# Kernel optimization log

Measured on AMD Instinct MI355X. Metric: run time of the kernel, lower is better.

Reference implementation:

```python
import jax, jax.numpy as jnp
import numpy as np

TOK_DIM = 512
POS_DIM = 512
N_HEADS = 16
HEAD_DIM = 64
D_MODEL = 1024
INNER = N_HEADS * HEAD_DIM
B, T = 4, 2048


def setup_inputs() -> dict:
    key = jax.random.key(0)
    ks = jax.random.split(key, 5)
    s = 0.02
    return {
        "x": jax.random.normal(ks[0], (B, T, TOK_DIM + POS_DIM), dtype=jnp.float32),
        "Wq": jax.random.normal(ks[1], (POS_DIM, INNER), dtype=jnp.float32) * s,
        "Wk": jax.random.normal(ks[2], (POS_DIM, INNER), dtype=jnp.float32) * s,
        "Wv": jax.random.normal(ks[3], (TOK_DIM, INNER), dtype=jnp.float32) * s,
        "Wo": jax.random.normal(ks[4], (INNER, D_MODEL), dtype=jnp.float32) * s,
    }


def reference(x, Wq, Wk, Wv, Wo):
    b, t, _ = x.shape
    x_tok = x[:, :, :TOK_DIM]
    x_pos = x[:, :, TOK_DIM:]
    # project and split heads: [B, H, T, Dh]
    q = (x_pos @ Wq).reshape(b, t, N_HEADS, HEAD_DIM).transpose(0, 2, 1, 3)
    k = (x_pos @ Wk).reshape(b, t, N_HEADS, HEAD_DIM).transpose(0, 2, 1, 3)
    v = (x_tok @ Wv).reshape(b, t, N_HEADS, HEAD_DIM).transpose(0, 2, 1, 3)
    att = jnp.einsum("bhqd,bhkd->bhqk", q, k) / jnp.sqrt(jnp.float32(HEAD_DIM))
    causal = jnp.tril(jnp.ones((t, t), dtype=bool))
    att = jnp.where(causal, att, -jnp.inf)
    att = jax.nn.softmax(att, axis=-1)
    out = jnp.einsum("bhqk,bhkd->bhqd", att, v)
    out = out.transpose(0, 2, 1, 3).reshape(b, t, INNER)
    return out @ Wo
```

## Files before the change

### kernel.cpp

```cpp
#include <hip/hip_runtime.h>
#include <stdint.h>


typedef unsigned short u16;
typedef __bf16 bf16;
typedef bf16 bf16x8 __attribute__((ext_vector_type(8)));
typedef u16 u16x8 __attribute__((ext_vector_type(8)));
typedef u16 u16x4 __attribute__((ext_vector_type(4)));
typedef float f32x4 __attribute__((ext_vector_type(4)));
typedef uint32_t u32x4 __attribute__((ext_vector_type(4)));

__device__ __forceinline__ u16 cvt_bf16(float f) {
  uint32_t u = __builtin_bit_cast(uint32_t, f);
  u += 0x7FFFu + ((u >> 16) & 1u);
  return (u16)(u >> 16);
}

__device__ __forceinline__ uint32_t pack2_bf16(float lo, float hi) {
  uint32_t a = __builtin_bit_cast(uint32_t, lo) + 0x8000u;
  uint32_t b = __builtin_bit_cast(uint32_t, hi) + 0x8000u;
  return __builtin_amdgcn_perm(b, a, 0x07060302u);
}

__device__ __forceinline__ f32x4 mfma_bf(bf16x8 a, bf16x8 b, f32x4 c) {
  return __builtin_amdgcn_mfma_f32_16x16x32_bf16(a, b, c, 0, 0, 0);
}

typedef __attribute__((address_space(1))) const uint32_t g_u32;
typedef __attribute__((address_space(3))) uint32_t l_u32;
__device__ __forceinline__ void gload16(const u16* g, u16* l) {
  __builtin_amdgcn_global_load_lds((g_u32*)g, (l_u32*)l, 16, 0, 0);
}

__global__ __launch_bounds__(256) void prep_x(
    const float* __restrict__ x, u16* __restrict__ xtok,
    u16* __restrict__ xpos) {
  int idx = blockIdx.x * 256 + threadIdx.x;
  int row = idx >> 8;
  int c4 = (idx & 255) * 4;
  float4 v = *(const float4*)(x + (size_t)row * 1024 + c4);
  u16x4 b = {cvt_bf16(v.x), cvt_bf16(v.y), cvt_bf16(v.z), cvt_bf16(v.w)};
  u16* dst = (c4 < 512) ? (xtok + (size_t)row * 512 + c4)
                        : (xpos + (size_t)row * 512 + c4 - 512);
  *(u16x4*)dst = b;
}

__global__ __launch_bounds__(256) void prep_w(
    const float* __restrict__ Wq, const float* __restrict__ Wk,
    const float* __restrict__ Wv, const float* __restrict__ Wo,
    u16* __restrict__ Wt, u16* __restrict__ WoT) {
  const int z = blockIdx.z;
  const float* src = (z == 0) ? Wq : (z == 1) ? Wk : (z == 2) ? Wv : Wo;
  const int K = (z == 3) ? 1024 : 512;
  u16* dst = (z == 3) ? WoT : (Wt + (size_t)z * 1024 * 512);
  const int k0 = blockIdx.y * 64, n0 = blockIdx.x * 64;
  if (k0 >= K) return;
  __shared__ u16 T[64][68];
  const int tid = threadIdx.x;
  const int r = tid >> 4, c = (tid & 15) * 4;
#pragma unroll
  for (int i = 0; i < 4; i++) {
    float4 v = *(const float4*)(src + (size_t)(k0 + r + i * 16) * 1024 + n0 + c);
    u16x4 b = {cvt_bf16(v.x), cvt_bf16(v.y), cvt_bf16(v.z), cvt_bf16(v.w)};
    *(u16x4*)&T[r + i * 16][c] = b;
  }
  __syncthreads();
#pragma unroll
  for (int i = 0; i < 4; i++) {
    int n = r + i * 16;
    u16x4 v;
#pragma unroll
    for (int j = 0; j < 4; j++) v[j] = T[c + j][n];
    *(u16x4*)(dst + (size_t)(n0 + n) * K + k0 + c) = v;
  }
}

__global__ __launch_bounds__(256) void gemm_qkv(
    const u16* __restrict__ xtok, const u16* __restrict__ xpos,
    const u16* __restrict__ Wt, u16* __restrict__ qkv,
    u16* __restrict__ vperm) {
  const int z = blockIdx.z;
  const u16* A = (z == 2) ? xtok : xpos;
  const u16* Bt = Wt + (size_t)z * 1024 * 512;
  u16* outp = qkv + (size_t)z * (64u * 2048u * 64u);
  const float osc = (z == 0) ? 0.18033688011112042f : 1.0f;

  const int m0 = blockIdx.y * 128;
  const int n0 = blockIdx.x * 128;
  const int tid = threadIdx.x;
  const int lane = tid & 63;
  const int w = tid >> 6;
  const int wm = (w & 1) * 64;
  const int wn = (w >> 1) * 64;
  const int mrow = lane & 15;
  const int quad = lane >> 4;

  __shared__ __align__(16) u16 Ash[128 * 32];
  __shared__ __align__(16) u16 Bsh[128 * 32];

  f32x4 acc[4][4];
#pragma unroll
  for (int i = 0; i < 4; i++)
#pragma unroll
    for (int j = 0; j < 4; j++) acc[i][j] = (f32x4){0.f, 0.f, 0.f, 0.f};

  const int sr = w * 16 + (lane >> 2);
  const int sc = (lane & 3) * 8;
  const u16* gA = A + (size_t)(m0 + sr) * 512 + sc;
  const u16* gB = Bt + (size_t)(n0 + sr) * 512 + sc;
  u16* lA = Ash + sr * 32 + sc;
  u16* lB = Bsh + sr * 32 + sc;

  for (int kb = 0; kb < 512; kb += 32) {
    __syncthreads();
    gload16(gA + kb, lA);
    gload16(gA + 64 * 512 + kb, lA + 64 * 32);
    gload16(gB + kb, lB);
    gload16(gB + 64 * 512 + kb, lB + 64 * 32);
    __syncthreads();

    bf16x8 af[4], bfr[4];
#pragma unroll
    for (int mi = 0; mi < 4; mi++)
      af[mi] = *(const bf16x8*)(Ash + (wm + mi * 16 + mrow) * 32 + quad * 8);
#pragma unroll
    for (int ni = 0; ni < 4; ni++)
      bfr[ni] = *(const bf16x8*)(Bsh + (wn + ni * 16 + mrow) * 32 + quad * 8);
#pragma unroll
    for (int mi = 0; mi < 4; mi++)
#pragma unroll
      for (int ni = 0; ni < 4; ni++)
        acc[mi][ni] = mfma_bf(af[mi], bfr[ni], acc[mi][ni]);
  }

  if (z != 2) {
#pragma unroll
    for (int mi = 0; mi < 4; mi++)
#pragma unroll
      for (int ni = 0; ni < 4; ni++)
#pragma unroll
        for (int r = 0; r < 4; r++) {
          int m = m0 + wm + mi * 16 + quad * 4 + r;
          int n = n0 + wn + ni * 16 + mrow;
          int bb = m >> 11, t = m & 2047;
          int h = n >> 6, d = n & 63;
          outp[(((size_t)(bb * 16 + h)) * 2048 + t) * 64 + d] =
              cvt_bf16(acc[mi][ni][r] * osc);
        }
  } else {
#pragma unroll
    for (int mi = 0; mi < 4; mi++)
#pragma unroll
      for (int ni = 0; ni < 4; ni++)
#pragma unroll
        for (int r = 0; r < 4; r++) {
          int m = m0 + wm + mi * 16 + quad * 4 + r;
          int n = n0 + wn + ni * 16 + mrow;
          int bb = m >> 11, t = m & 2047;
          int h = n >> 6, d = n & 63;
          int k6 = t & 63;
          int pos = (k6 & 32) + ((k6 >> 4) & 1) * 4 + ((k6 >> 2) & 3) * 8 +
                    (k6 & 3);
          vperm[(((size_t)(bb * 16 + h)) * 64 + d) * 2048 + (t & ~63) + pos] =
              cvt_bf16(acc[mi][ni][r]);
        }
  }
}

__global__ __launch_bounds__(256, 2) void attn(
    const u16* __restrict__ qkv, const u16* __restrict__ vperm,
    u16* __restrict__ aout) {
  const int bh = blockIdx.x;
  const int sp = blockIdx.y;
  const int bb = bh >> 4, h = bh & 15;
  const u16* Qp = qkv + (size_t)bh * (2048 * 64);
  const u16* Kp = qkv + (size_t)(64 + bh) * (2048 * 64);
  const u16* Vp = vperm + (size_t)bh * (64 * 2048);

  __shared__ __align__(16) u16 Ksh0[64 * 32], Ksh1[64 * 32];
  __shared__ __align__(16) u16 Vsh0[64 * 32], Vsh1[64 * 32];
  __shared__ __align__(16) u16 Osh[4][32][72];

  const int tid = threadIdx.x;
  const int lane = tid & 63;
  const int w = tid >> 6;
  const int mrow = lane & 15;
  const int quad = lane >> 4;
  const int srow = w * 16 + (lane >> 2);
  const int sc = (lane & 3) * 8;

  const u16x8 onesu = {0x3F80, 0x3F80, 0x3F80, 0x3F80,
                       0x3F80, 0x3F80, 0x3F80, 0x3F80};
  const bf16x8 ones = __builtin_bit_cast(bf16x8, onesu);

  const u16* kgb = Kp + (size_t)srow * 64 + sc;
  const u16* vgb = Vp + (size_t)srow * 2048 + sc;

  for (int half = 0; half < 2; ++half) {
    const int qt = (half == 0) ? sp : 15 - sp;
    const int q0 = qt * 128;
    const int nk = 2 * qt + 2;
    const int qw = q0 + w * 32;

    const u16* qbase = Qp + (size_t)(qw + mrow) * 64 + quad * 8;
    const bf16x8 qf00 = *(const bf16x8*)qbase;
    const bf16x8 qf01 = *(const bf16x8*)(qbase + 32);
    const bf16x8 qf10 = *(const bf16x8*)(qbase + 16 * 64);
    const bf16x8 qf11 = *(const bf16x8*)(qbase + 16 * 64 + 32);

    f32x4 o[2][4], ol[2];
#pragma unroll
    for (int g = 0; g < 2; ++g) {
#pragma unroll
      for (int dt = 0; dt < 4; ++dt) o[g][dt] = (f32x4){0.f, 0.f, 0.f, 0.f};
      ol[g] = (f32x4){0.f, 0.f, 0.f, 0.f};
    }

    u16x8 ka0 = *(const u16x8*)kgb;
    u16x8 ka1 = *(const u16x8*)(kgb + 32);
    u16x8 va0 = *(const u16x8*)vgb;
    u16x8 va1 = *(const u16x8*)(vgb + 32);

    for (int it = 0; it < nk; ++it) {
      __syncthreads();
      *(u16x8*)(Ksh0 + srow * 32 + sc) = ka0;
      *(u16x8*)(Ksh1 + srow * 32 + sc) = ka1;
      *(u16x8*)(Vsh0 + srow * 32 + sc) = va0;
      *(u16x8*)(Vsh1 + srow * 32 + sc) = va1;
      __syncthreads();

      if (it + 1 < nk) {
        const int kn = (it + 1) * 64;
        ka0 = *(const u16x8*)(kgb + (size_t)kn * 64);
        ka1 = *(const u16x8*)(kgb + (size_t)kn * 64 + 32);
        va0 = *(const u16x8*)(vgb + kn);
        va1 = *(const u16x8*)(vgb + kn + 32);
      }

      const int k0 = it * 64;
      if (k0 > qw + 31) continue;

      f32x4 s[2][4];
#pragma unroll
      for (int nt = 0; nt < 4; ++nt) {
        bf16x8 kf0 = *(const bf16x8*)(Ksh0 + (nt * 16 + mrow) * 32 + quad * 8);
        bf16x8 kf1 = *(const bf16x8*)(Ksh1 + (nt * 16 + mrow) * 32 + quad * 8);
        f32x4 z0 = (f32x4){0.f, 0.f, 0.f, 0.f};
        z0 = mfma_bf(kf0, qf00, z0);
        s[0][nt] = mfma_bf(kf1, qf01, z0);
        f32x4 z1 = (f32x4){0.f, 0.f, 0.f, 0.f};
        z1 = mfma_bf(kf0, qf10, z1);
        s[1][nt] = mfma_bf(kf1, qf11, z1);
      }

      if (k0 + 63 > qw) {
#pragma unroll
        for (int g = 0; g < 2; ++g)
#pragma unroll
          for (int nt = 0; nt < 4; ++nt)
#pragma unroll
            for (int r = 0; r < 4; ++r)
              if (k0 + nt * 16 + quad * 4 + r > qw + g * 16 + mrow)
                s[g][nt][r] = -1e30f;
      }
#pragma unroll
      for (int g = 0; g < 2; ++g)
#pragma unroll
        for (int nt = 0; nt < 4; ++nt)
#pragma unroll
          for (int r = 0; r < 4; ++r)
            s[g][nt][r] = __builtin_amdgcn_exp2f(s[g][nt][r]);

      bf16x8 pf[2][2];
#pragma unroll
      for (int g = 0; g < 2; ++g) {
        u32x4 pw0 = {pack2_bf16(s[g][0][0], s[g][0][1]),
                     pack2_bf16(s[g][0][2], s[g][0][3]),
                     pack2_bf16(s[g][1][0], s[g][1][1]),
                     pack2_bf16(s[g][1][2], s[g][1][3])};
        u32x4 pw1 = {pack2_bf16(s[g][2][0], s[g][2][1]),
                     pack2_bf16(s[g][2][2], s[g][2][3]),
                     pack2_bf16(s[g][3][0], s[g][3][1]),
                     pack2_bf16(s[g][3][2], s[g][3][3])};
        pf[g][0] = __builtin_bit_cast(bf16x8, pw0);
        pf[g][1] = __builtin_bit_cast(bf16x8, pw1);
        ol[g] = mfma_bf(ones, pf[g][0], ol[g]);
        ol[g] = mfma_bf(ones, pf[g][1], ol[g]);
      }

#pragma unroll
      for (int dt = 0; dt < 4; ++dt) {
        bf16x8 vf0 = *(const bf16x8*)(Vsh0 + (dt * 16 + mrow) * 32 + quad * 8);
        bf16x8 vf1 = *(const bf16x8*)(Vsh1 + (dt * 16 + mrow) * 32 + quad * 8);
        o[0][dt] = mfma_bf(vf0, pf[0][0], o[0][dt]);
        o[0][dt] = mfma_bf(vf1, pf[0][1], o[0][dt]);
        o[1][dt] = mfma_bf(vf0, pf[1][0], o[1][dt]);
        o[1][dt] = mfma_bf(vf1, pf[1][1], o[1][dt]);
      }
    }

#pragma unroll
    for (int g = 0; g < 2; ++g) {
      const float inv = 1.f / ol[g][0];
#pragma unroll
      for (int dt = 0; dt < 4; ++dt)
#pragma unroll
        for (int r = 0; r < 4; ++r)
          Osh[w][g * 16 + mrow][dt * 16 + quad * 4 + r] =
              cvt_bf16(o[g][dt][r] * inv);
    }
#pragma unroll
    for (int p = 0; p < 4; ++p) {
      int ql = (lane >> 3) + 8 * p;
      int ch = lane & 7;
      u16x8 v = *(const u16x8*)&Osh[w][ql][ch * 8];
      int t = q0 + w * 32 + ql;
      *(u16x8*)(aout + ((size_t)(bb * 2048 + t)) * 1024 + h * 64 + ch * 8) = v;
    }
  }
}

__global__ __launch_bounds__(256) void gemm_out(
    const u16* __restrict__ Am, const u16* __restrict__ WoT,
    float* __restrict__ out) {
  const int m0 = blockIdx.y * 128;
  const int n0 = blockIdx.x * 128;
  const int tid = threadIdx.x;
  const int lane = tid & 63;
  const int w = tid >> 6;
  const int wm = (w & 1) * 64;
  const int wn = (w >> 1) * 64;
  const int mrow = lane & 15;
  const int quad = lane >> 4;

  __shared__ __align__(16) u16 Ash[128 * 32];
  __shared__ __align__(16) u16 Bsh[128 * 32];

  f32x4 acc[4][4];
#pragma unroll
  for (int i = 0; i < 4; i++)
#pragma unroll
    for (int j = 0; j < 4; j++) acc[i][j] = (f32x4){0.f, 0.f, 0.f, 0.f};

  const int sr = w * 16 + (lane >> 2);
  const int sc = (lane & 3) * 8;
  const u16* gA = Am + (size_t)(m0 + sr) * 1024 + sc;
  const u16* gB = WoT + (size_t)(n0 + sr) * 1024 + sc;
  u16* lA = Ash + sr * 32 + sc;
  u16* lB = Bsh + sr * 32 + sc;

  for (int kb = 0; kb < 1024; kb += 32) {
    __syncthreads();
    gload16(gA + kb, lA);
    gload16(gA + 64 * 1024 + kb, lA + 64 * 32);
    gload16(gB + kb, lB);
    gload16(gB + 64 * 1024 + kb, lB + 64 * 32);
    __syncthreads();

    bf16x8 af[4], bfr[4];
#pragma unroll
    for (int mi = 0; mi < 4; mi++)
      af[mi] = *(const bf16x8*)(Ash + (wm + mi * 16 + mrow) * 32 + quad * 8);
#pragma unroll
    for (int ni = 0; ni < 4; ni++)
      bfr[ni] = *(const bf16x8*)(Bsh + (wn + ni * 16 + mrow) * 32 + quad * 8);
#pragma unroll
    for (int mi = 0; mi < 4; mi++)
#pragma unroll
      for (int ni = 0; ni < 4; ni++)
        acc[mi][ni] = mfma_bf(af[mi], bfr[ni], acc[mi][ni]);
  }

#pragma unroll
  for (int mi = 0; mi < 4; mi++)
#pragma unroll
    for (int ni = 0; ni < 4; ni++)
#pragma unroll
      for (int r = 0; r < 4; r++) {
        int m = m0 + wm + mi * 16 + quad * 4 + r;
        int n = n0 + wn + ni * 16 + mrow;
        out[(size_t)m * 1024 + n] = acc[mi][ni][r];
      }
}

extern "C" void kernel_launch(void* const* d_in, const int* in_sizes, int n_in,
                              void* d_out, int out_size, void* d_ws, size_t ws_size,
                              hipStream_t stream) {
  const float* x  = (const float*)d_in[0];
  const float* Wq = (const float*)d_in[1];
  const float* Wk = (const float*)d_in[2];
  const float* Wv = (const float*)d_in[3];
  const float* Wo = (const float*)d_in[4];

  u16* qkv   = (u16*)d_ws;
  u16* vperm = qkv + (size_t)3 * 64 * 2048 * 64;
  u16* aout  = vperm + (size_t)64 * 64 * 2048;
  u16* xtok  = aout + (size_t)8192 * 1024;
  u16* xpos  = xtok + (size_t)8192 * 512;
  u16* Wt    = xpos + (size_t)8192 * 512;
  u16* WoT   = Wt + (size_t)3 * 1024 * 512;
  float* out = (float*)d_out;

  prep_x<<<dim3(8192), dim3(256), 0, stream>>>(x, xtok, xpos);
  prep_w<<<dim3(16, 16, 4), dim3(256), 0, stream>>>(Wq, Wk, Wv, Wo, Wt, WoT);
  gemm_qkv<<<dim3(8, 64, 3), dim3(256), 0, stream>>>(xtok, xpos, Wt, qkv, vperm);
  attn<<<dim3(64, 8), dim3(256), 0, stream>>>(qkv, vperm, aout);
  gemm_out<<<dim3(8, 64), dim3(256), 0, stream>>>(aout, WoT, out);
}
```

Measured before the change: 215.3 us.

## Replace QKV and output GEMMs with 256x256 pipelined, swizzled 8-wave GEMM core

Both projection GEMMs now share a 256x256-tile core run by 512 threads. It uses K-step 64, double-buffered LDS with XOR-swizzled layout, and interleaved global-to-LDS loads issued between MFMA phases. Raw s_barrier and s_waitcnt calls plus setprio are used in place of __syncthreads. The goal is more data reuse per tile, fewer LDS bank conflicts, and load latency hidden behind compute. In exchange it uses 128KB LDS per block, heavy register use from 32 accumulators, and fewer blocks (384 for QKV, 128 for the output GEMM), which may leave CUs idle on the smaller GEMM.

```diff
diff --git a/kernel.cpp b/kernel.cpp
--- a/kernel.cpp
+++ b/kernel.cpp
@@ -75,7 +75,113 @@
   }
 }
 
-__global__ __launch_bounds__(256) void gemm_qkv(
+
+#define LDA(P, S) { const u16* bp_ = rA + (P)*16384 + (S)*8192;              \
+  af[0][0] = *(const bf16x8*)(bp_ + 0*1024 + colx0);                         \
+  af[0][1] = *(const bf16x8*)(bp_ + 0*1024 + colx1);                         \
+  af[1][0] = *(const bf16x8*)(bp_ + 1*1024 + colx0);                         \
+  af[1][1] = *(const bf16x8*)(bp_ + 1*1024 + colx1);                         \
+  af[2][0] = *(const bf16x8*)(bp_ + 2*1024 + colx0);                         \
+  af[2][1] = *(const bf16x8*)(bp_ + 2*1024 + colx1);                         \
+  af[3][0] = *(const bf16x8*)(bp_ + 3*1024 + colx0);                         \
+  af[3][1] = *(const bf16x8*)(bp_ + 3*1024 + colx1); }
+
+#define LDB(P, S, NB) { const u16* bp_ = rB + (P)*16384 + (S)*8192;          \
+  bf[(NB)+0][0] = *(const bf16x8*)(bp_ + 0*1024 + colx0);                    \
+  bf[(NB)+0][1] = *(const bf16x8*)(bp_ + 0*1024 + colx1);                    \
+  bf[(NB)+1][0] = *(const bf16x8*)(bp_ + 1*1024 + colx0);                    \
+  bf[(NB)+1][1] = *(const bf16x8*)(bp_ + 1*1024 + colx1); }
+
+#define MM1(M_, N_, J_) { f32x4 c_ = acc[M_][N_];                            \
+  c_ = mfma_bf(af[J_][0], bf[N_][0], c_);                                    \
+  c_ = mfma_bf(af[J_][1], bf[N_][1], c_);                                    \
+  acc[M_][N_] = c_; }
+
+#define MM(MB, NB) MM1((MB)+0,(NB)+0,0) MM1((MB)+0,(NB)+1,0)                 \
+                   MM1((MB)+1,(NB)+0,1) MM1((MB)+1,(NB)+1,1)                 \
+                   MM1((MB)+2,(NB)+0,2) MM1((MB)+2,(NB)+1,2)                 \
+                   MM1((MB)+3,(NB)+0,3) MM1((MB)+3,(NB)+1,3)
+
+#define STA(P, S, KT) { const u16* s_ = gA + (size_t)(S)*64*Kd + (KT)*64;    \
+  u16* d_ = lA + (P)*16384 + (S)*8192;                                       \
+  gload16(s_, d_); gload16(s_ + (size_t)128*Kd, d_ + 4096); }
+
+#define STB(P, S, KT) { const u16* s_ = gB + (size_t)(S)*32*Kd + (KT)*64;    \
+  u16* d_ = lB + (P)*16384 + (S)*8192;                                       \
+  gload16(s_, d_); gload16(s_ + (size_t)128*Kd, d_ + 4096); }
+
+#define PH_MID  asm volatile("" ::: "memory"); __builtin_amdgcn_s_barrier(); \
+  asm volatile("s_waitcnt lgkmcnt(0)" ::: "memory");                         \
+  __builtin_amdgcn_s_setprio(1);
+
+#define PH_END  __builtin_amdgcn_s_setprio(0);                               \
+  asm volatile("" ::: "memory"); __builtin_amdgcn_s_barrier();
+
+#define PH_END_VM  __builtin_amdgcn_s_setprio(0);                            \
+  asm volatile("s_waitcnt vmcnt(6)" ::: "memory");                           \
+  asm volatile("" ::: "memory"); __builtin_amdgcn_s_barrier();
+
+template <int Kd>
+__device__ __forceinline__ void gemm256_core(
+    const u16* __restrict__ Aptr, const u16* __restrict__ Bptr,
+    int m0, int n0, u16* smem, f32x4 (&acc)[8][4]) {
+  constexpr int NKT = Kd / 64;
+  constexpr int NI = NKT / 2;
+  const int tid = threadIdx.x;
+  const int lane = tid & 63;
+  const int mrow = lane & 15, quad = lane >> 4;
+  const int w = tid >> 6, wm2 = w >> 2, wn4 = w & 3;
+
+  u16* As = smem;
+  u16* Bs = smem + 32768;
+
+  const int lrs = tid >> 3, sp8 = tid & 7;
+  const int slog = sp8 ^ (lrs & 7);
+  const u16* gA = Aptr + (size_t)(m0 + (lrs & 63)) * Kd + slog * 8;
+  const u16* gB =
+      Bptr + (size_t)(n0 + ((lrs >> 5) << 6) + (lrs & 31)) * Kd + slog * 8;
+  u16* lA = As + tid * 8;
+  u16* lB = Bs + tid * 8;
+
+  const int colx0 = (quad * 8) ^ ((mrow & 7) * 8);
+  const int colx1 = (32 + quad * 8) ^ ((mrow & 7) * 8);
+  const u16* rA = As + (wm2 * 64 + mrow) * 64;
+  const u16* rB = Bs + (wn4 * 32 + mrow) * 64;
+
+  bf16x8 af[4][2], bf[4][2];
+
+  STA(0, 0, 0) STB(0, 0, 0) STB(0, 1, 0) STA(0, 1, 0)
+  STA(1, 0, 1) STB(1, 0, 1) STB(1, 1, 1)
+  asm volatile("s_waitcnt vmcnt(6)" ::: "memory");
+  asm volatile("" ::: "memory");
+  __builtin_amdgcn_s_barrier();
+
+  for (int i = 0; i < NI; ++i) {
+    const int kt1 = 2 * i + 1;
+    const int kt2 = (2 * i + 2 < NKT) ? 2 * i + 2 : NKT - 1;
+    const int kt3 = (2 * i + 3 < NKT) ? 2 * i + 3 : NKT - 1;
+    LDA(0, 0) LDB(0, 0, 0) STA(1, 1, kt1)
+    PH_MID MM(0, 0) PH_END
+    LDB(0, 1, 2) STA(0, 0, kt2)
+    PH_MID MM(0, 2) PH_END
+    LDA(0, 1) STB(0, 0, kt2)
+    PH_MID MM(4, 2) PH_END
+    STB(0, 1, kt2)
+    PH_MID MM(4, 0) PH_END_VM
+    LDA(1, 0) LDB(1, 0, 0) STA(0, 1, kt2)
+    PH_MID MM(0, 0) PH_END
+    LDB(1, 1, 2) STA(1, 0, kt3)
+    PH_MID MM(0, 2) PH_END
+    LDA(1, 1) STB(1, 0, kt3)
+    PH_MID MM(4, 2) PH_END
+    STB(1, 1, kt3)
+    PH_MID MM(4, 0) PH_END_VM
+  }
+  asm volatile("s_waitcnt vmcnt(0)" ::: "memory");
+  __builtin_amdgcn_s_barrier();
+}
+
+__global__ __launch_bounds__(512, 2) void gemm_qkv256(
     const u16* __restrict__ xtok, const u16* __restrict__ xpos,
     const u16* __restrict__ Wt, u16* __restrict__ qkv,
     u16* __restrict__ vperm) {
@@ -84,64 +190,31 @@
   const u16* Bt = Wt + (size_t)z * 1024 * 512;
   u16* outp = qkv + (size_t)z * (64u * 2048u * 64u);
   const float osc = (z == 0) ? 0.18033688011112042f : 1.0f;
-
-  const int m0 = blockIdx.y * 128;
-  const int n0 = blockIdx.x * 128;
+  const int m0 = blockIdx.y * 256, n0 = blockIdx.x * 256;
+
+  __shared__ __align__(16) u16 smem[65536];
+  f32x4 acc[8][4];
+#pragma unroll
+  for (int i = 0; i < 8; i++)
+#pragma unroll
+    for (int j = 0; j < 4; j++) acc[i][j] = (f32x4){0.f, 0.f, 0.f, 0.f};
+
+  gemm256_core<512>(A, Bt, m0, n0, smem, acc);
+
   const int tid = threadIdx.x;
   const int lane = tid & 63;
-  const int w = tid >> 6;
-  const int wm = (w & 1) * 64;
-  const int wn = (w >> 1) * 64;
-  const int mrow = lane & 15;
-  const int quad = lane >> 4;
-
-  __shared__ __align__(16) u16 Ash[128 * 32];
-  __shared__ __align__(16) u16 Bsh[128 * 32];
-
-  f32x4 acc[4][4];
-#pragma unroll
-  for (int i = 0; i < 4; i++)
-#pragma unroll
-    for (int j = 0; j < 4; j++) acc[i][j] = (f32x4){0.f, 0.f, 0.f, 0.f};
-
-  const int sr = w * 16 + (lane >> 2);
-  const int sc = (lane & 3) * 8;
-  const u16* gA = A + (size_t)(m0 + sr) * 512 + sc;
-  const u16* gB = Bt + (size_t)(n0 + sr) * 512 + sc;
-  u16* lA = Ash + sr * 32 + sc;
-  u16* lB = Bsh + sr * 32 + sc;
-
-  for (int kb = 0; kb < 512; kb += 32) {
-    __syncthreads();
-    gload16(gA + kb, lA);
-    gload16(gA + 64 * 512 + kb, lA + 64 * 32);
-    gload16(gB + kb, lB);
-    gload16(gB + 64 * 512 + kb, lB + 64 * 32);
-    __syncthreads();
-
-    bf16x8 af[4], bfr[4];
-#pragma unroll
-    for (int mi = 0; mi < 4; mi++)
-      af[mi] = *(const bf16x8*)(Ash + (wm + mi * 16 + mrow) * 32 + quad * 8);
-#pragma unroll
-    for (int ni = 0; ni < 4; ni++)
-      bfr[ni] = *(const bf16x8*)(Bsh + (wn + ni * 16 + mrow) * 32 + quad * 8);
-#pragma unroll
-    for (int mi = 0; mi < 4; mi++)
+  const int mrow = lane & 15, quad = lane >> 4;
+  const int w = tid >> 6, wm2 = w >> 2, wn4 = w & 3;
+
+  if (z != 2) {
+#pragma unroll
+    for (int mi = 0; mi < 8; mi++)
 #pragma unroll
       for (int ni = 0; ni < 4; ni++)
-        acc[mi][ni] = mfma_bf(af[mi], bfr[ni], acc[mi][ni]);
-  }
-
-  if (z != 2) {
-#pragma unroll
-    for (int mi = 0; mi < 4; mi++)
-#pragma unroll
-      for (int ni = 0; ni < 4; ni++)
 #pragma unroll
         for (int r = 0; r < 4; r++) {
-          int m = m0 + wm + mi * 16 + quad * 4 + r;
-          int n = n0 + wn + ni * 16 + mrow;
+          int m = m0 + wm2 * 128 + mi * 16 + quad * 4 + r;
+          int n = n0 + wn4 * 64 + ni * 16 + mrow;
           int bb = m >> 11, t = m & 2047;
           int h = n >> 6, d = n & 63;
           outp[(((size_t)(bb * 16 + h)) * 2048 + t) * 64 + d] =
@@ -149,13 +222,13 @@
         }
   } else {
 #pragma unroll
-    for (int mi = 0; mi < 4; mi++)
+    for (int mi = 0; mi < 8; mi++)
 #pragma unroll
       for (int ni = 0; ni < 4; ni++)
 #pragma unroll
         for (int r = 0; r < 4; r++) {
-          int m = m0 + wm + mi * 16 + quad * 4 + r;
-          int n = n0 + wn + ni * 16 + mrow;
+          int m = m0 + wm2 * 128 + mi * 16 + quad * 4 + r;
+          int n = n0 + wn4 * 64 + ni * 16 + mrow;
           int bb = m >> 11, t = m & 2047;
           int h = n >> 6, d = n & 63;
           int k6 = t & 63;
@@ -165,6 +238,37 @@
               cvt_bf16(acc[mi][ni][r]);
         }
   }
+}
+
+__global__ __launch_bounds__(512, 2) void gemm_out256(
+    const u16* __restrict__ Am, const u16* __restrict__ WoT,
+    float* __restrict__ out) {
+  const int m0 = blockIdx.y * 256, n0 = blockIdx.x * 256;
+
+  __shared__ __align__(16) u16 smem[65536];
+  f32x4 acc[8][4];
+#pragma unroll
+  for (int i = 0; i < 8; i++)
+#pragma unroll
+    for (int j = 0; j < 4; j++) acc[i][j] = (f32x4){0.f, 0.f, 0.f, 0.f};
+
+  gemm256_core<1024>(Am, WoT, m0, n0, smem, acc);
+
+  const int tid = threadIdx.x;
+  const int lane = tid & 63;
+  const int mrow = lane & 15, quad = lane >> 4;
+  const int w = tid >> 6, wm2 = w >> 2, wn4 = w & 3;
+
+#pragma unroll
+  for (int mi = 0; mi < 8; mi++)
+#pragma unroll
+    for (int ni = 0; ni < 4; ni++)
+#pragma unroll
+      for (int r = 0; r < 4; r++) {
+        int m = m0 + wm2 * 128 + mi * 16 + quad * 4 + r;
+        int n = n0 + wn4 * 64 + ni * 16 + mrow;
+        out[(size_t)m * 1024 + n] = acc[mi][ni][r];
+      }
 }
 
 __global__ __launch_bounds__(256, 2) void attn(
@@ -320,69 +424,6 @@
   }
 }
 
-__global__ __launch_bounds__(256) void gemm_out(
-    const u16* __restrict__ Am, const u16* __restrict__ WoT,
-    float* __restrict__ out) {
-  const int m0 = blockIdx.y * 128;
-  const int n0 = blockIdx.x * 128;
-  const int tid = threadIdx.x;
-  const int lane = tid & 63;
-  const int w = tid >> 6;
-  const int wm = (w & 1) * 64;
-  const int wn = (w >> 1) * 64;
-  const int mrow = lane & 15;
-  const int quad = lane >> 4;
-
-  __shared__ __align__(16) u16 Ash[128 * 32];
-  __shared__ __align__(16) u16 Bsh[128 * 32];
-
-  f32x4 acc[4][4];
-#pragma unroll
-  for (int i = 0; i < 4; i++)
-#pragma unroll
-    for (int j = 0; j < 4; j++) acc[i][j] = (f32x4){0.f, 0.f, 0.f, 0.f};
-
-  const int sr = w * 16 + (lane >> 2);
-  const int sc = (lane & 3) * 8;
-  const u16* gA = Am + (size_t)(m0 + sr) * 1024 + sc;
-  const u16* gB = WoT + (size_t)(n0 + sr) * 1024 + sc;
-  u16* lA = Ash + sr * 32 + sc;
-  u16* lB = Bsh + sr * 32 + sc;
-
-  for (int kb = 0; kb < 1024; kb += 32) {
-    __syncthreads();
-    gload16(gA + kb, lA);
-    gload16(gA + 64 * 1024 + kb, lA + 64 * 32);
-    gload16(gB + kb, lB);
-    gload16(gB + 64 * 1024 + kb, lB + 64 * 32);
-    __syncthreads();
-
-    bf16x8 af[4], bfr[4];
-#pragma unroll
-    for (int mi = 0; mi < 4; mi++)
-      af[mi] = *(const bf16x8*)(Ash + (wm + mi * 16 + mrow) * 32 + quad * 8);
-#pragma unroll
-    for (int ni = 0; ni < 4; ni++)
-      bfr[ni] = *(const bf16x8*)(Bsh + (wn + ni * 16 + mrow) * 32 + quad * 8);
-#pragma unroll
-    for (int mi = 0; mi < 4; mi++)
-#pragma unroll
-      for (int ni = 0; ni < 4; ni++)
-        acc[mi][ni] = mfma_bf(af[mi], bfr[ni], acc[mi][ni]);
-  }
-
-#pragma unroll
-  for (int mi = 0; mi < 4; mi++)
-#pragma unroll
-    for (int ni = 0; ni < 4; ni++)
-#pragma unroll
-      for (int r = 0; r < 4; r++) {
-        int m = m0 + wm + mi * 16 + quad * 4 + r;
-        int n = n0 + wn + ni * 16 + mrow;
-        out[(size_t)m * 1024 + n] = acc[mi][ni][r];
-      }
-}
-
 extern "C" void kernel_launch(void* const* d_in, const int* in_sizes, int n_in,
                               void* d_out, int out_size, void* d_ws, size_t ws_size,
                               hipStream_t stream) {
@@ -403,7 +444,7 @@
 
   prep_x<<<dim3(8192), dim3(256), 0, stream>>>(x, xtok, xpos);
   prep_w<<<dim3(16, 16, 4), dim3(256), 0, stream>>>(Wq, Wk, Wv, Wo, Wt, WoT);
-  gemm_qkv<<<dim3(8, 64, 3), dim3(256), 0, stream>>>(xtok, xpos, Wt, qkv, vperm);
+  gemm_qkv256<<<dim3(4, 32, 3), dim3(512), 0, stream>>>(xtok, xpos, Wt, qkv, vperm);
   attn<<<dim3(64, 8), dim3(256), 0, stream>>>(qkv, vperm, aout);
-  gemm_out<<<dim3(8, 64), dim3(256), 0, stream>>>(aout, WoT, out);
-}
+  gemm_out256<<<dim3(4, 32), dim3(512), 0, stream>>>(aout, WoT, out);
+}
```

Result: faster. 206.9 us (-3.9%).
